# Kernel optimization log

Hardware: AMD Instinct MI355X
Metric: run time of the kernel (lower is better)

Reference implementation:

```python
import jax, jax.numpy as jnp
import numpy as np

PAD = 0  # padding token id; its embedding row is zero (padding_idx)


def setup_inputs() -> dict:
    key = jax.random.key(0)
    k1, k2, k3 = jax.random.split(key, 3)
    HOPS, VOCAB, D = 3, 50257, 128
    B, M, S = 32, 512, 6        # batch, memory slots, tokens per slot
    T, L = 128, 64              # trees per example, tokens per (flattened) tree
    # hop+1 embedding tables, normal(0, 0.1) like the torch init
    C = 0.1 * jax.random.normal(k1, (HOPS + 1, VOCAB, D), dtype=jnp.float32)
    C = C.at[:, PAD].set(0.0)   # padding_idx row = 0
    story = jax.random.randint(k2, (B, M, S), 0, VOCAB, dtype=jnp.int32)
    kb_tokens = jax.random.randint(k3, (B, T, L), 0, VOCAB, dtype=jnp.int32)
    return {"C": C, "story": story, "kb_tokens": kb_tokens}


def reference(C, story, kb_tokens):
    # C: [hops+1, V, D]; story: [B, M, S]; kb_tokens: [B, T, L]
    hops = C.shape[0] - 1
    B = story.shape[0]
    D = C.shape[-1]
    u = jnp.zeros((B, D), dtype=C.dtype)
    for hop in range(hops):
        # key memory: story slots (sum over tokens) + tree memories (sum over
        # all subtree tokens == dfs recursive sum, since PAD embeds to zero)
        m_story_A = jnp.take(C[hop], story, axis=0).sum(axis=2)       # [B,M,D]
        tree_A = jnp.take(C[hop], kb_tokens, axis=0).sum(axis=2)      # [B,T,D]
        m_A = jnp.concatenate([m_story_A, tree_A], axis=1)            # [B,M+T,D]
        prob = jax.nn.softmax(jnp.einsum("bmd,bd->bm", m_A, u), axis=1)
        # value memory with next-hop table
        m_story_C = jnp.take(C[hop + 1], story, axis=0).sum(axis=2)
        tree_C = jnp.take(C[hop + 1], kb_tokens, axis=0).sum(axis=2)
        m_C = jnp.concatenate([m_story_C, tree_C], axis=1)
        o_k = jnp.einsum("bm,bmd->bd", prob, m_C)
        u = u + o_k
    return u
```

## Files before the change

kernel.cpp:

```cpp
#include <hip/hip_runtime.h>
#include <math.h>

constexpr int HOPS  = 3;
constexpr int VOCAB = 50257;
constexpr int DIM   = 128;
constexpr int NB    = 32;
constexpr int NM    = 512;
constexpr int NS    = 6;
constexpr int NT    = 128;
constexpr int NL    = 64;
constexpr int SLOTS = NM + NT;
constexpr size_t TS = (size_t)VOCAB * DIM;
constexpr size_t TABSTRIDE = (size_t)NB * SLOTS * DIM;

constexpr size_t CH_ELEMS = (size_t)VOCAB * 3 * DIM;
constexpr int NE8 = (int)(CH_ELEMS / 8);

typedef _Float16 half8 __attribute__((ext_vector_type(8)));
typedef _Float16 half4 __attribute__((ext_vector_type(4)));

constexpr int CONV_BLOCKS   = 2048;
constexpr int GATHER_BLOCKS = 2048;

__global__ __launch_bounds__(256) void convert_k(
    const float* __restrict__ C, _Float16* __restrict__ Ch)
{
    for (int e8 = blockIdx.x * 256 + threadIdx.x; e8 < NE8; e8 += CONV_BLOCKS * 256) {
        const size_t base = (size_t)e8 * 8;
        const size_t v    = base / 384;
        const int    rem  = (int)(base % 384);
        const int    tab  = rem >> 7;
        const int    d    = rem & 127;
        const float* src = C + (size_t)(1 + tab) * TS + v * DIM + d;
        float4 f0 = *(const float4*)(src);
        float4 f1 = *(const float4*)(src + 4);
        half8 h;
        h[0]=(_Float16)f0.x; h[1]=(_Float16)f0.y; h[2]=(_Float16)f0.z; h[3]=(_Float16)f0.w;
        h[4]=(_Float16)f1.x; h[5]=(_Float16)f1.y; h[6]=(_Float16)f1.z; h[7]=(_Float16)f1.w;
        *(half8*)(Ch + base) = h;
    }
}

__global__ __launch_bounds__(256) void gather_k(
    const _Float16* __restrict__ Ch, const int* __restrict__ story,
    const int* __restrict__ kb, _Float16* __restrict__ msum)
{
    const int wave = threadIdx.x >> 6, lane = threadIdx.x & 63;
    const int q = lane >> 4, l16 = lane & 15;

    if (wave < 2) {
        const int g = blockIdx.x * 2 + wave;
        const int b = g >> 7, tr = g & (NT - 1);

        const int tok = kb[(size_t)g * NL + lane];

        float a0[8] = {0,0,0,0,0,0,0,0};
        float a1[8] = {0,0,0,0,0,0,0,0};
        float a2[8] = {0,0,0,0,0,0,0,0};

        #pragma unroll
        for (int i = 0; i < 16; ++i) {
            const int s = __shfl(tok, (lane & 48) + i);
            const _Float16* p = Ch + (size_t)s * (3 * DIM) + l16 * 8;
            half8 v0 = *(const half8*)(p);
            half8 v1 = *(const half8*)(p + DIM);
            half8 v2 = *(const half8*)(p + 2 * DIM);
            #pragma unroll
            for (int j = 0; j < 8; ++j) {
                a0[j] = fmaf((float)v0[j], 1.0f, a0[j]);
                a1[j] = fmaf((float)v1[j], 1.0f, a1[j]);
                a2[j] = fmaf((float)v2[j], 1.0f, a2[j]);
            }
        }
        #pragma unroll
        for (int j = 0; j < 8; ++j) {
            a0[j] += __shfl_xor(a0[j], 16); a0[j] += __shfl_xor(a0[j], 32);
            a1[j] += __shfl_xor(a1[j], 16); a1[j] += __shfl_xor(a1[j], 32);
            a2[j] += __shfl_xor(a2[j], 16); a2[j] += __shfl_xor(a2[j], 32);
        }
        if (q == 0) {
            half8 h0, h1, h2;
            #pragma unroll
            for (int j = 0; j < 8; ++j) {
                h0[j] = (_Float16)a0[j]; h1[j] = (_Float16)a1[j]; h2[j] = (_Float16)a2[j];
            }
            const size_t o = ((size_t)b * SLOTS + NM + tr) * DIM + l16 * 8;
            *(half8*)(msum + o)                 = h0;
            *(half8*)(msum + o + TABSTRIDE)     = h1;
            *(half8*)(msum + o + 2 * TABSTRIDE) = h2;
        }
    } else {
        const int wbase = blockIdx.x * 8 + (wave - 2) * 4;
        const int* sidx = story + (size_t)wbase * NS;
        const int tokv = (lane < 4 * NS) ? sidx[lane] : 0;

        const int g = wbase + q;
        const int b = g >> 9, slot = g & (NM - 1);

        float a0[8] = {0,0,0,0,0,0,0,0};
        float a1[8] = {0,0,0,0,0,0,0,0};
        float a2[8] = {0,0,0,0,0,0,0,0};

        #pragma unroll
        for (int i = 0; i < NS; ++i) {
            const int s = __shfl(tokv, q * NS + i);
            const _Float16* p = Ch + (size_t)s * (3 * DIM) + l16 * 8;
            half8 v0 = *(const half8*)(p);
            half8 v1 = *(const half8*)(p + DIM);
            half8 v2 = *(const half8*)(p + 2 * DIM);
            #pragma unroll
            for (int j = 0; j < 8; ++j) {
                a0[j] = fmaf((float)v0[j], 1.0f, a0[j]);
                a1[j] = fmaf((float)v1[j], 1.0f, a1[j]);
                a2[j] = fmaf((float)v2[j], 1.0f, a2[j]);
            }
        }
        half8 h0, h1, h2;
        #pragma unroll
        for (int j = 0; j < 8; ++j) {
            h0[j] = (_Float16)a0[j]; h1[j] = (_Float16)a1[j]; h2[j] = (_Float16)a2[j];
        }
        const size_t o = ((size_t)b * SLOTS + slot) * DIM + l16 * 8;
        *(half8*)(msum + o)                 = h0;
        *(half8*)(msum + o + TABSTRIDE)     = h1;
        *(half8*)(msum + o + 2 * TABSTRIDE) = h2;
    }
}

__global__ __launch_bounds__(1024) void hops_fused(
    const _Float16* __restrict__ msum, float* __restrict__ out)
{
    const int b = blockIdx.x, t = threadIdx.x;
    const int rg = t >> 4, l16 = t & 15, wv = t >> 6, ln = t & 63;
    __shared__ float u_s[DIM];
    __shared__ float probs[SLOTS];
    __shared__ float part[64][DIM + 4];
    __shared__ float red[16];

    const _Float16* base = msum + (size_t)b * SLOTS * DIM;
    const int doff = l16 * 8;

    half8 vc[10];

    {
        float acc[8] = {0,0,0,0,0,0,0,0};
        #pragma unroll
        for (int r = 0; r < 10; ++r)
            vc[r] = *(const half8*)(base + (size_t)(rg + 64 * r) * DIM + doff);
        #pragma unroll
        for (int r = 0; r < 10; ++r) {
            #pragma unroll
            for (int j = 0; j < 8; ++j) acc[j] += (float)vc[r][j];
        }
        #pragma unroll
        for (int j = 0; j < 8; ++j) part[rg][doff + j] = acc[j];
        __syncthreads();
        if (t < DIM) {
            float s = 0.f;
            #pragma unroll
            for (int r = 0; r < 64; ++r) s += part[r][t];
            u_s[t] = s * (1.f / SLOTS);
        }
        __syncthreads();
    }

    #pragma unroll
    for (int hop = 1; hop < HOPS; ++hop) {
        float u_reg[8];
        #pragma unroll
        for (int j = 0; j < 8; ++j) u_reg[j] = u_s[doff + j];

        #pragma unroll
        for (int r = 0; r < 10; ++r) {
            const int m = rg + 64 * r;
            float d = 0.f;
            #pragma unroll
            for (int j = 0; j < 8; ++j) d = fmaf((float)vc[r][j], u_reg[j], d);
            d += __shfl_xor(d, 1); d += __shfl_xor(d, 2);
            d += __shfl_xor(d, 4); d += __shfl_xor(d, 8);
            if (l16 == 0) probs[m] = d;
        }
        __syncthreads();

        float s0 = (t < SLOTS) ? probs[t] : -INFINITY;
        float lmax = s0;
        #pragma unroll
        for (int off = 32; off > 0; off >>= 1) lmax = fmaxf(lmax, __shfl_xor(lmax, off));
        if (ln == 0) red[wv] = lmax;
        __syncthreads();
        lmax = red[0];
        #pragma unroll
        for (int r = 1; r < 16; ++r) lmax = fmaxf(lmax, red[r]);
        __syncthreads();
        float e0 = (t < SLOTS) ? expf(s0 - lmax) : 0.f;
        if (t < SLOTS) probs[t] = e0;
        float lsum = e0;
        #pragma unroll
        for (int off = 32; off > 0; off >>= 1) lsum += __shfl_xor(lsum, off);
        if (ln == 0) red[wv] = lsum;
        __syncthreads();
        float tot = red[0];
        #pragma unroll
        for (int r = 1; r < 16; ++r) tot += red[r];
        const float inv = 1.0f / tot;

        const _Float16* mC = base + (size_t)hop * TABSTRIDE;
        float acc[8] = {0,0,0,0,0,0,0,0};
        #pragma unroll
        for (int r = 0; r < 10; ++r) {
            const int m = rg + 64 * r;
            vc[r] = *(const half8*)(mC + (size_t)m * DIM + doff);
            const float p = probs[m];
            #pragma unroll
            for (int j = 0; j < 8; ++j) acc[j] = fmaf(p, (float)vc[r][j], acc[j]);
        }
        __syncthreads();
        #pragma unroll
        for (int j = 0; j < 8; ++j) part[rg][doff + j] = acc[j];
        __syncthreads();
        if (t < DIM) {
            float s = 0.f;
            #pragma unroll
            for (int r = 0; r < 64; ++r) s += part[r][t];
            u_s[t] += s * inv;
        }
        __syncthreads();
    }

    if (t < DIM) out[b * DIM + t] = u_s[t];
}

extern "C" void kernel_launch(void* const* d_in, const int* in_sizes, int n_in,
                              void* d_out, int out_size, void* d_ws, size_t ws_size,
                              hipStream_t stream) {
    const float* C     = (const float*)d_in[0];
    const int*   story = (const int*)d_in[1];
    const int*   kb    = (const int*)d_in[2];
    float*       out   = (float*)d_out;

    _Float16* Ch   = (_Float16*)d_ws;
    _Float16* msum = Ch + CH_ELEMS;

    convert_k<<<CONV_BLOCKS, 256, 0, stream>>>(C, Ch);
    gather_k<<<GATHER_BLOCKS, 256, 0, stream>>>(Ch, story, kb, msum);
    hops_fused<<<NB, 1024, 0, stream>>>(msum, out);
}
```

Baseline: 212.4 us.

## Fuse convert, gather and hop kernels into one cooperative kernel with grid syncs

Merges the three launches into one cooperative kernel of 256 blocks of 1024 threads, separated by grid-wide barriers. Conversion, gather of trees and story slots, and the hop attention phase run in sequence, with the last phase on 32 blocks only. The aim is to remove inter-kernel launch gaps. In exchange it lowers block-level parallelism, adds grid sync costs, and raises register pressure from sharing one kernel at 1024 threads.

```diff
diff --git a/kernel.cpp b/kernel.cpp
--- a/kernel.cpp
+++ b/kernel.cpp
@@ -1,5 +1,8 @@
 #include <hip/hip_runtime.h>
+#include <hip/hip_cooperative_groups.h>
 #include <math.h>
+
+namespace cg = cooperative_groups;
 
 constexpr int HOPS  = 3;
 constexpr int VOCAB = 50257;
@@ -17,15 +20,20 @@
 constexpr int NE8 = (int)(CH_ELEMS / 8);
 
 typedef _Float16 half8 __attribute__((ext_vector_type(8)));
-typedef _Float16 half4 __attribute__((ext_vector_type(4)));
-
-constexpr int CONV_BLOCKS   = 2048;
-constexpr int GATHER_BLOCKS = 2048;
-
-__global__ __launch_bounds__(256) void convert_k(
-    const float* __restrict__ C, _Float16* __restrict__ Ch)
+
+constexpr int GRID = 256;
+
+__global__ __launch_bounds__(1024) void fused_all(
+    const float* __restrict__ C, const int* __restrict__ story,
+    const int* __restrict__ kb, _Float16* __restrict__ Ch,
+    _Float16* __restrict__ msum, float* __restrict__ out)
 {
-    for (int e8 = blockIdx.x * 256 + threadIdx.x; e8 < NE8; e8 += CONV_BLOCKS * 256) {
+    cg::grid_group grid = cg::this_grid();
+    const int t = threadIdx.x;
+    const int wave = t >> 6, lane = t & 63;
+    const int q = lane >> 4, l16 = lane & 15;
+
+    for (int e8 = blockIdx.x * 1024 + t; e8 < NE8; e8 += GRID * 1024) {
         const size_t base = (size_t)e8 * 8;
         const size_t v    = base / 384;
         const int    rem  = (int)(base % 384);
@@ -39,17 +47,11 @@
         h[4]=(_Float16)f1.x; h[5]=(_Float16)f1.y; h[6]=(_Float16)f1.z; h[7]=(_Float16)f1.w;
         *(half8*)(Ch + base) = h;
     }
-}
-
-__global__ __launch_bounds__(256) void gather_k(
-    const _Float16* __restrict__ Ch, const int* __restrict__ story,
-    const int* __restrict__ kb, _Float16* __restrict__ msum)
-{
-    const int wave = threadIdx.x >> 6, lane = threadIdx.x & 63;
-    const int q = lane >> 4, l16 = lane & 15;
-
-    if (wave < 2) {
-        const int g = blockIdx.x * 2 + wave;
+
+    grid.sync();
+
+    {
+        const int g = blockIdx.x * 16 + wave;
         const int b = g >> 7, tr = g & (NT - 1);
 
         const int tok = kb[(size_t)g * NL + lane];
@@ -89,17 +91,17 @@
             *(half8*)(msum + o + TABSTRIDE)     = h1;
             *(half8*)(msum + o + 2 * TABSTRIDE) = h2;
         }
-    } else {
-        const int wbase = blockIdx.x * 8 + (wave - 2) * 4;
+
+        const int wbase = blockIdx.x * 64 + wave * 4;
         const int* sidx = story + (size_t)wbase * NS;
         const int tokv = (lane < 4 * NS) ? sidx[lane] : 0;
 
-        const int g = wbase + q;
-        const int b = g >> 9, slot = g & (NM - 1);
-
-        float a0[8] = {0,0,0,0,0,0,0,0};
-        float a1[8] = {0,0,0,0,0,0,0,0};
-        float a2[8] = {0,0,0,0,0,0,0,0};
+        const int gs = wbase + q;
+        const int bs = gs >> 9, slot = gs & (NM - 1);
+
+        float b0[8] = {0,0,0,0,0,0,0,0};
+        float b1[8] = {0,0,0,0,0,0,0,0};
+        float b2[8] = {0,0,0,0,0,0,0,0};
 
         #pragma unroll
         for (int i = 0; i < NS; ++i) {
@@ -110,124 +112,124 @@
             half8 v2 = *(const half8*)(p + 2 * DIM);
             #pragma unroll
             for (int j = 0; j < 8; ++j) {
-                a0[j] = fmaf((float)v0[j], 1.0f, a0[j]);
-                a1[j] = fmaf((float)v1[j], 1.0f, a1[j]);
-                a2[j] = fmaf((float)v2[j], 1.0f, a2[j]);
+                b0[j] = fmaf((float)v0[j], 1.0f, b0[j]);
+                b1[j] = fmaf((float)v1[j], 1.0f, b1[j]);
+                b2[j] = fmaf((float)v2[j], 1.0f, b2[j]);
             }
         }
         half8 h0, h1, h2;
         #pragma unroll
         for (int j = 0; j < 8; ++j) {
-            h0[j] = (_Float16)a0[j]; h1[j] = (_Float16)a1[j]; h2[j] = (_Float16)a2[j];
-        }
-        const size_t o = ((size_t)b * SLOTS + slot) * DIM + l16 * 8;
+            h0[j] = (_Float16)b0[j]; h1[j] = (_Float16)b1[j]; h2[j] = (_Float16)b2[j];
+        }
+        const size_t o = ((size_t)bs * SLOTS + slot) * DIM + l16 * 8;
         *(half8*)(msum + o)                 = h0;
         *(half8*)(msum + o + TABSTRIDE)     = h1;
         *(half8*)(msum + o + 2 * TABSTRIDE) = h2;
     }
-}
-
-__global__ __launch_bounds__(1024) void hops_fused(
-    const _Float16* __restrict__ msum, float* __restrict__ out)
-{
-    const int b = blockIdx.x, t = threadIdx.x;
-    const int rg = t >> 4, l16 = t & 15, wv = t >> 6, ln = t & 63;
-    __shared__ float u_s[DIM];
-    __shared__ float probs[SLOTS];
-    __shared__ float part[64][DIM + 4];
-    __shared__ float red[16];
-
-    const _Float16* base = msum + (size_t)b * SLOTS * DIM;
-    const int doff = l16 * 8;
-
-    half8 vc[10];
-
-    {
-        float acc[8] = {0,0,0,0,0,0,0,0};
-        #pragma unroll
-        for (int r = 0; r < 10; ++r)
-            vc[r] = *(const half8*)(base + (size_t)(rg + 64 * r) * DIM + doff);
-        #pragma unroll
-        for (int r = 0; r < 10; ++r) {
-            #pragma unroll
-            for (int j = 0; j < 8; ++j) acc[j] += (float)vc[r][j];
-        }
-        #pragma unroll
-        for (int j = 0; j < 8; ++j) part[rg][doff + j] = acc[j];
-        __syncthreads();
-        if (t < DIM) {
-            float s = 0.f;
-            #pragma unroll
-            for (int r = 0; r < 64; ++r) s += part[r][t];
-            u_s[t] = s * (1.f / SLOTS);
-        }
-        __syncthreads();
+
+    grid.sync();
+
+    if (blockIdx.x < NB) {
+        const int b = blockIdx.x;
+        const int rg = t >> 4, wv = t >> 6, ln = t & 63;
+        __shared__ float u_s[DIM];
+        __shared__ float probs[SLOTS];
+        __shared__ float part[64][DIM + 4];
+        __shared__ float red[16];
+
+        const _Float16* base = msum + (size_t)b * SLOTS * DIM;
+        const int doff = l16 * 8;
+
+        half8 vc[10];
+
+        {
+            float acc[8] = {0,0,0,0,0,0,0,0};
+            #pragma unroll
+            for (int r = 0; r < 10; ++r)
+                vc[r] = *(const half8*)(base + (size_t)(rg + 64 * r) * DIM + doff);
+            #pragma unroll
+            for (int r = 0; r < 10; ++r) {
+                #pragma unroll
+                for (int j = 0; j < 8; ++j) acc[j] += (float)vc[r][j];
+            }
+            #pragma unroll
+            for (int j = 0; j < 8; ++j) part[rg][doff + j] = acc[j];
+            __syncthreads();
+            if (t < DIM) {
+                float s = 0.f;
+                #pragma unroll
+                for (int r = 0; r < 64; ++r) s += part[r][t];
+                u_s[t] = s * (1.f / SLOTS);
+            }
+            __syncthreads();
+        }
+
+        #pragma unroll
+        for (int hop = 1; hop < HOPS; ++hop) {
+            float u_reg[8];
+            #pragma unroll
+            for (int j = 0; j < 8; ++j) u_reg[j] = u_s[doff + j];
+
+            #pragma unroll
+            for (int r = 0; r < 10; ++r) {
+                const int m = rg + 64 * r;
+                float d = 0.f;
+                #pragma unroll
+                for (int j = 0; j < 8; ++j) d = fmaf((float)vc[r][j], u_reg[j], d);
+                d += __shfl_xor(d, 1); d += __shfl_xor(d, 2);
+                d += __shfl_xor(d, 4); d += __shfl_xor(d, 8);
+                if (l16 == 0) probs[m] = d;
+            }
+            __syncthreads();
+
+            float s0 = (t < SLOTS) ? probs[t] : -INFINITY;
+            float lmax = s0;
+            #pragma unroll
+            for (int off = 32; off > 0; off >>= 1) lmax = fmaxf(lmax, __shfl_xor(lmax, off));
+            if (ln == 0) red[wv] = lmax;
+            __syncthreads();
+            lmax = red[0];
+            #pragma unroll
+            for (int r = 1; r < 16; ++r) lmax = fmaxf(lmax, red[r]);
+            __syncthreads();
+            float e0 = (t < SLOTS) ? expf(s0 - lmax) : 0.f;
+            if (t < SLOTS) probs[t] = e0;
+            float lsum = e0;
+            #pragma unroll
+            for (int off = 32; off > 0; off >>= 1) lsum += __shfl_xor(lsum, off);
+            if (ln == 0) red[wv] = lsum;
+            __syncthreads();
+            float tot = red[0];
+            #pragma unroll
+            for (int r = 1; r < 16; ++r) tot += red[r];
+            const float inv = 1.0f / tot;
+
+            const _Float16* mC = base + (size_t)hop * TABSTRIDE;
+            float acc[8] = {0,0,0,0,0,0,0,0};
+            #pragma unroll
+            for (int r = 0; r < 10; ++r) {
+                const int m = rg + 64 * r;
+                vc[r] = *(const half8*)(mC + (size_t)m * DIM + doff);
+                const float p = probs[m];
+                #pragma unroll
+                for (int j = 0; j < 8; ++j) acc[j] = fmaf(p, (float)vc[r][j], acc[j]);
+            }
+            __syncthreads();
+            #pragma unroll
+            for (int j = 0; j < 8; ++j) part[rg][doff + j] = acc[j];
+            __syncthreads();
+            if (t < DIM) {
+                float s = 0.f;
+                #pragma unroll
+                for (int r = 0; r < 64; ++r) s += part[r][t];
+                u_s[t] += s * inv;
+            }
+            __syncthreads();
+        }
+
+        if (t < DIM) out[b * DIM + t] = u_s[t];
     }
-
-    #pragma unroll
-    for (int hop = 1; hop < HOPS; ++hop) {
-        float u_reg[8];
-        #pragma unroll
-        for (int j = 0; j < 8; ++j) u_reg[j] = u_s[doff + j];
-
-        #pragma unroll
-        for (int r = 0; r < 10; ++r) {
-            const int m = rg + 64 * r;
-            float d = 0.f;
-            #pragma unroll
-            for (int j = 0; j < 8; ++j) d = fmaf((float)vc[r][j], u_reg[j], d);
-            d += __shfl_xor(d, 1); d += __shfl_xor(d, 2);
-            d += __shfl_xor(d, 4); d += __shfl_xor(d, 8);
-            if (l16 == 0) probs[m] = d;
-        }
-        __syncthreads();
-
-        float s0 = (t < SLOTS) ? probs[t] : -INFINITY;
-        float lmax = s0;
-        #pragma unroll
-        for (int off = 32; off > 0; off >>= 1) lmax = fmaxf(lmax, __shfl_xor(lmax, off));
-        if (ln == 0) red[wv] = lmax;
-        __syncthreads();
-        lmax = red[0];
-        #pragma unroll
-        for (int r = 1; r < 16; ++r) lmax = fmaxf(lmax, red[r]);
-        __syncthreads();
-        float e0 = (t < SLOTS) ? expf(s0 - lmax) : 0.f;
-        if (t < SLOTS) probs[t] = e0;
-        float lsum = e0;
-        #pragma unroll
-        for (int off = 32; off > 0; off >>= 1) lsum += __shfl_xor(lsum, off);
-        if (ln == 0) red[wv] = lsum;
-        __syncthreads();
-        float tot = red[0];
-        #pragma unroll
-        for (int r = 1; r < 16; ++r) tot += red[r];
-        const float inv = 1.0f / tot;
-
-        const _Float16* mC = base + (size_t)hop * TABSTRIDE;
-        float acc[8] = {0,0,0,0,0,0,0,0};
-        #pragma unroll
-        for (int r = 0; r < 10; ++r) {
-            const int m = rg + 64 * r;
-            vc[r] = *(const half8*)(mC + (size_t)m * DIM + doff);
-            const float p = probs[m];
-            #pragma unroll
-            for (int j = 0; j < 8; ++j) acc[j] = fmaf(p, (float)vc[r][j], acc[j]);
-        }
-        __syncthreads();
-        #pragma unroll
-        for (int j = 0; j < 8; ++j) part[rg][doff + j] = acc[j];
-        __syncthreads();
-        if (t < DIM) {
-            float s = 0.f;
-            #pragma unroll
-            for (int r = 0; r < 64; ++r) s += part[r][t];
-            u_s[t] += s * inv;
-        }
-        __syncthreads();
-    }
-
-    if (t < DIM) out[b * DIM + t] = u_s[t];
 }
 
 extern "C" void kernel_launch(void* const* d_in, const int* in_sizes, int n_in,
@@ -241,7 +243,8 @@
     _Float16* Ch   = (_Float16*)d_ws;
     _Float16* msum = Ch + CH_ELEMS;
 
-    convert_k<<<CONV_BLOCKS, 256, 0, stream>>>(C, Ch);
-    gather_k<<<GATHER_BLOCKS, 256, 0, stream>>>(Ch, story, kb, msum);
-    hops_fused<<<NB, 1024, 0, stream>>>(msum, out);
+    void* args[] = { (void*)&C, (void*)&story, (void*)&kb,
+                     (void*)&Ch, (void*)&msum, (void*)&out };
+    hipLaunchCooperativeKernel((void*)fused_all, dim3(GRID), dim3(1024),
+                               args, 0, stream);
 }
```

Measured after the change: 298.9 us. 1.41x slower.

## Split tree and story gathers into separate blocks, halving per-wave tree work

Applied to the files above, without the earlier changes.

The gather kernel previously mixed 2 tree waves (16 tokens per lane group each) with 2 story waves in every block, so the tree waves ran much longer and the story waves idled. Now tree blocks and story blocks are separate. Each tree is split across two waves of 32 tokens, and the two partial sums are combined through shared memory. This is meant to balance wave runtimes and double the parallelism on the long tree gathers, at the cost of a block sync and LDS traffic for the extra reduction.

```diff
diff --git a/kernel.cpp b/kernel.cpp
--- a/kernel.cpp
+++ b/kernel.cpp
@@ -17,10 +17,11 @@
 constexpr int NE8 = (int)(CH_ELEMS / 8);
 
 typedef _Float16 half8 __attribute__((ext_vector_type(8)));
-typedef _Float16 half4 __attribute__((ext_vector_type(4)));
-
-constexpr int CONV_BLOCKS   = 2048;
-constexpr int GATHER_BLOCKS = 2048;
+
+constexpr int CONV_BLOCKS  = 2048;
+constexpr int TREE_BLOCKS  = NB * NT / 2;
+constexpr int STORY_BLOCKS = NB * NM / 16;
+constexpr int GATHER_BLOCKS = TREE_BLOCKS + STORY_BLOCKS;
 
 __global__ __launch_bounds__(256) void convert_k(
     const float* __restrict__ C, _Float16* __restrict__ Ch)
@@ -48,19 +49,21 @@
     const int wave = threadIdx.x >> 6, lane = threadIdx.x & 63;
     const int q = lane >> 4, l16 = lane & 15;
 
-    if (wave < 2) {
-        const int g = blockIdx.x * 2 + wave;
+    if (blockIdx.x < TREE_BLOCKS) {
+        __shared__ float tred[4][3][DIM];
+        const int tl = wave >> 1, half = wave & 1;
+        const int g = blockIdx.x * 2 + tl;
         const int b = g >> 7, tr = g & (NT - 1);
 
-        const int tok = kb[(size_t)g * NL + lane];
+        const int tok = (lane < 32) ? kb[(size_t)g * NL + half * 32 + lane] : 0;
 
         float a0[8] = {0,0,0,0,0,0,0,0};
         float a1[8] = {0,0,0,0,0,0,0,0};
         float a2[8] = {0,0,0,0,0,0,0,0};
 
         #pragma unroll
-        for (int i = 0; i < 16; ++i) {
-            const int s = __shfl(tok, (lane & 48) + i);
+        for (int i = 0; i < 8; ++i) {
+            const int s = __shfl(tok, q * 8 + i);
             const _Float16* p = Ch + (size_t)s * (3 * DIM) + l16 * 8;
             half8 v0 = *(const half8*)(p);
             half8 v1 = *(const half8*)(p + DIM);
@@ -79,10 +82,22 @@
             a2[j] += __shfl_xor(a2[j], 16); a2[j] += __shfl_xor(a2[j], 32);
         }
         if (q == 0) {
+            #pragma unroll
+            for (int j = 0; j < 8; ++j) {
+                tred[wave][0][l16 * 8 + j] = a0[j];
+                tred[wave][1][l16 * 8 + j] = a1[j];
+                tred[wave][2][l16 * 8 + j] = a2[j];
+            }
+        }
+        __syncthreads();
+        if (half == 0 && q == 0) {
             half8 h0, h1, h2;
             #pragma unroll
             for (int j = 0; j < 8; ++j) {
-                h0[j] = (_Float16)a0[j]; h1[j] = (_Float16)a1[j]; h2[j] = (_Float16)a2[j];
+                const int d = l16 * 8 + j;
+                h0[j] = (_Float16)(tred[wave][0][d] + tred[wave + 1][0][d]);
+                h1[j] = (_Float16)(tred[wave][1][d] + tred[wave + 1][1][d]);
+                h2[j] = (_Float16)(tred[wave][2][d] + tred[wave + 1][2][d]);
             }
             const size_t o = ((size_t)b * SLOTS + NM + tr) * DIM + l16 * 8;
             *(half8*)(msum + o)                 = h0;
@@ -90,7 +105,8 @@
             *(half8*)(msum + o + 2 * TABSTRIDE) = h2;
         }
     } else {
-        const int wbase = blockIdx.x * 8 + (wave - 2) * 4;
+        const int sb = blockIdx.x - TREE_BLOCKS;
+        const int wbase = sb * 16 + wave * 4;
         const int* sidx = story + (size_t)wbase * NS;
         const int tokv = (lane < 4 * NS) ? sidx[lane] : 0;
 
```

After: 213.8 us. About the same (+0.6%).

## Partition fp16 embedding copy into 8 dimension slices for cache-local gather

Applied to the files above, without the earlier changes.

The converted fp16 table is re-laid out as 8 slices of 16 dims each ([x][vocab][table][16]). The gather is split so that each block handles one dimension slice, giving each slice about 4.8 MB of table to work on, so it can stay resident in cache. Partial sums are reduced through shared memory. The trade-off is 8x more blocks, shorter 32-byte accesses per token, extra shared-memory reductions and syncs, and redundant token index loads.

```diff
diff --git a/kernel.cpp b/kernel.cpp
--- a/kernel.cpp
+++ b/kernel.cpp
@@ -13,17 +13,21 @@
 constexpr size_t TS = (size_t)VOCAB * DIM;
 constexpr size_t TABSTRIDE = (size_t)NB * SLOTS * DIM;
 
+constexpr int NG = 8;
+constexpr int GW = 16;
 constexpr size_t CH_ELEMS = (size_t)VOCAB * 3 * DIM;
 constexpr int NE8 = (int)(CH_ELEMS / 8);
 
 typedef _Float16 half8 __attribute__((ext_vector_type(8)));
-typedef _Float16 half4 __attribute__((ext_vector_type(4)));
-
-constexpr int CONV_BLOCKS   = 2048;
-constexpr int GATHER_BLOCKS = 2048;
+
+constexpr int CONV_BLOCKS = 2048;
+constexpr int TREE_B2   = NB * NT * NG / 4;
+constexpr int STORY_GB  = (NB * NM + 11) / 12;
+constexpr int STORY_B2  = STORY_GB * NG;
+constexpr int GATHER_B2 = TREE_B2 + STORY_B2;
 
 __global__ __launch_bounds__(256) void convert_k(
-    const float* __restrict__ C, _Float16* __restrict__ Ch)
+    const float* __restrict__ C, _Float16* __restrict__ Ch2)
 {
     for (int e8 = blockIdx.x * 256 + threadIdx.x; e8 < NE8; e8 += CONV_BLOCKS * 256) {
         const size_t base = (size_t)e8 * 8;
@@ -31,99 +35,118 @@
         const int    rem  = (int)(base % 384);
         const int    tab  = rem >> 7;
         const int    d    = rem & 127;
+        const int    x    = d >> 4;
+        const int    dl   = d & 15;
         const float* src = C + (size_t)(1 + tab) * TS + v * DIM + d;
         float4 f0 = *(const float4*)(src);
         float4 f1 = *(const float4*)(src + 4);
         half8 h;
         h[0]=(_Float16)f0.x; h[1]=(_Float16)f0.y; h[2]=(_Float16)f0.z; h[3]=(_Float16)f0.w;
         h[4]=(_Float16)f1.x; h[5]=(_Float16)f1.y; h[6]=(_Float16)f1.z; h[7]=(_Float16)f1.w;
-        *(half8*)(Ch + base) = h;
+        const size_t out = (((size_t)x * VOCAB + v) * 3 + tab) * GW + dl;
+        *(half8*)(Ch2 + out) = h;
     }
 }
 
 __global__ __launch_bounds__(256) void gather_k(
-    const _Float16* __restrict__ Ch, const int* __restrict__ story,
+    const _Float16* __restrict__ Ch2, const int* __restrict__ story,
     const int* __restrict__ kb, _Float16* __restrict__ msum)
 {
+    __shared__ float shm [4][54][17];
+    __shared__ float shm2[4][3][16];
+
     const int wave = threadIdx.x >> 6, lane = threadIdx.x & 63;
-    const int q = lane >> 4, l16 = lane & 15;
-
-    if (wave < 2) {
-        const int g = blockIdx.x * 2 + wave;
+    const int x = blockIdx.x & 7;
+    const _Float16* gbase = Ch2 + (size_t)x * VOCAB * (3 * GW);
+
+    if (blockIdx.x < TREE_B2) {
+        const int g = (blockIdx.x >> 3) * 4 + wave;
         const int b = g >> 7, tr = g & (NT - 1);
 
         const int tok = kb[(size_t)g * NL + lane];
 
-        float a0[8] = {0,0,0,0,0,0,0,0};
-        float a1[8] = {0,0,0,0,0,0,0,0};
-        float a2[8] = {0,0,0,0,0,0,0,0};
-
-        #pragma unroll
-        for (int i = 0; i < 16; ++i) {
-            const int s = __shfl(tok, (lane & 48) + i);
-            const _Float16* p = Ch + (size_t)s * (3 * DIM) + l16 * 8;
-            half8 v0 = *(const half8*)(p);
-            half8 v1 = *(const half8*)(p + DIM);
-            half8 v2 = *(const half8*)(p + 2 * DIM);
+        const int p = lane >> 1, oct = lane & 1;
+        const int tabL = p % 3, kL = p / 3;
+
+        float acc[8] = {0,0,0,0,0,0,0,0};
+        #pragma unroll
+        for (int r = 0; r < 7; ++r) {
+            const int ti = 10 * r + kL;
+            int s = __shfl(tok, ti & 63);
+            if (ti >= 64 || p >= 30) s = 0;
+            const _Float16* ptr = gbase + ((size_t)s * 3 + tabL) * GW + oct * 8;
+            half8 v = *(const half8*)ptr;
+            #pragma unroll
+            for (int j = 0; j < 8; ++j) acc[j] += (float)v[j];
+        }
+        if (p < 30) {
+            #pragma unroll
+            for (int j = 0; j < 8; ++j) shm[wave][p][oct * 8 + j] = acc[j];
+        }
+        __syncthreads();
+        if (lane < 48) {
+            const int tab2 = lane >> 4, d2 = lane & 15;
+            float s = 0.f;
+            #pragma unroll
+            for (int k = 0; k < 10; ++k) s += shm[wave][3 * k + tab2][d2];
+            shm2[wave][tab2][d2] = s;
+        }
+        __syncthreads();
+        if (lane < 6) {
+            const int tab3 = lane >> 1, oct3 = lane & 1;
+            half8 h;
+            #pragma unroll
+            for (int j = 0; j < 8; ++j) h[j] = (_Float16)shm2[wave][tab3][oct3 * 8 + j];
+            const size_t o = ((size_t)b * SLOTS + NM + tr) * DIM + x * GW + oct3 * 8;
+            *(half8*)(msum + o + (size_t)tab3 * TABSTRIDE) = h;
+        }
+    } else {
+        const int gb = (blockIdx.x - TREE_B2) >> 3;
+        const int s0 = gb * 12 + wave * 3;
+        const int rem = NB * NM - s0;
+        const int nv = rem < 0 ? 0 : (rem < 3 ? rem : 3);
+
+        const int tokv = (lane < nv * NS && lane < 18)
+                       ? story[(size_t)s0 * NS + lane] : 0;
+
+        const int p = lane;
+        const int tabL = p % 3, tkL = (p / 3) % 6, slL = p / 18;
+        int s = 0;
+        if (p < 54) s = __shfl(tokv, slL * NS + tkL);
+
+        const _Float16* ptr = gbase + ((size_t)s * 3 + tabL) * GW;
+        half8 v0 = *(const half8*)(ptr);
+        half8 v1 = *(const half8*)(ptr + 8);
+        if (p < 54) {
             #pragma unroll
             for (int j = 0; j < 8; ++j) {
-                a0[j] = fmaf((float)v0[j], 1.0f, a0[j]);
-                a1[j] = fmaf((float)v1[j], 1.0f, a1[j]);
-                a2[j] = fmaf((float)v2[j], 1.0f, a2[j]);
+                shm[wave][p][j]     = (float)v0[j];
+                shm[wave][p][8 + j] = (float)v1[j];
             }
         }
         #pragma unroll
-        for (int j = 0; j < 8; ++j) {
-            a0[j] += __shfl_xor(a0[j], 16); a0[j] += __shfl_xor(a0[j], 32);
-            a1[j] += __shfl_xor(a1[j], 16); a1[j] += __shfl_xor(a1[j], 32);
-            a2[j] += __shfl_xor(a2[j], 16); a2[j] += __shfl_xor(a2[j], 32);
-        }
-        if (q == 0) {
-            half8 h0, h1, h2;
-            #pragma unroll
-            for (int j = 0; j < 8; ++j) {
-                h0[j] = (_Float16)a0[j]; h1[j] = (_Float16)a1[j]; h2[j] = (_Float16)a2[j];
+        for (int s3 = 0; s3 < 3; ++s3) {
+            __syncthreads();
+            if (lane < 48) {
+                const int tab2 = lane >> 4, d2 = lane & 15;
+                float sum = 0.f;
+                #pragma unroll
+                for (int t = 0; t < NS; ++t)
+                    sum += shm[wave][s3 * 18 + t * 3 + tab2][d2];
+                shm2[wave][tab2][d2] = sum;
             }
-            const size_t o = ((size_t)b * SLOTS + NM + tr) * DIM + l16 * 8;
-            *(half8*)(msum + o)                 = h0;
-            *(half8*)(msum + o + TABSTRIDE)     = h1;
-            *(half8*)(msum + o + 2 * TABSTRIDE) = h2;
-        }
-    } else {
-        const int wbase = blockIdx.x * 8 + (wave - 2) * 4;
-        const int* sidx = story + (size_t)wbase * NS;
-        const int tokv = (lane < 4 * NS) ? sidx[lane] : 0;
-
-        const int g = wbase + q;
-        const int b = g >> 9, slot = g & (NM - 1);
-
-        float a0[8] = {0,0,0,0,0,0,0,0};
-        float a1[8] = {0,0,0,0,0,0,0,0};
-        float a2[8] = {0,0,0,0,0,0,0,0};
-
-        #pragma unroll
-        for (int i = 0; i < NS; ++i) {
-            const int s = __shfl(tokv, q * NS + i);
-            const _Float16* p = Ch + (size_t)s * (3 * DIM) + l16 * 8;
-            half8 v0 = *(const half8*)(p);
-            half8 v1 = *(const half8*)(p + DIM);
-            half8 v2 = *(const half8*)(p + 2 * DIM);
-            #pragma unroll
-            for (int j = 0; j < 8; ++j) {
-                a0[j] = fmaf((float)v0[j], 1.0f, a0[j]);
-                a1[j] = fmaf((float)v1[j], 1.0f, a1[j]);
-                a2[j] = fmaf((float)v2[j], 1.0f, a2[j]);
+            __syncthreads();
+            if (lane < 6 && s3 < nv) {
+                const int tab3 = lane >> 1, oct3 = lane & 1;
+                const int sg = s0 + s3;
+                const int bb = sg >> 9, sl = sg & (NM - 1);
+                half8 h;
+                #pragma unroll
+                for (int j = 0; j < 8; ++j) h[j] = (_Float16)shm2[wave][tab3][oct3 * 8 + j];
+                const size_t o = ((size_t)bb * SLOTS + sl) * DIM + x * GW + oct3 * 8;
+                *(half8*)(msum + o + (size_t)tab3 * TABSTRIDE) = h;
             }
         }
-        half8 h0, h1, h2;
-        #pragma unroll
-        for (int j = 0; j < 8; ++j) {
-            h0[j] = (_Float16)a0[j]; h1[j] = (_Float16)a1[j]; h2[j] = (_Float16)a2[j];
-        }
-        const size_t o = ((size_t)b * SLOTS + slot) * DIM + l16 * 8;
-        *(half8*)(msum + o)                 = h0;
-        *(half8*)(msum + o + TABSTRIDE)     = h1;
-        *(half8*)(msum + o + 2 * TABSTRIDE) = h2;
     }
 }
 
@@ -238,10 +261,10 @@
     const int*   kb    = (const int*)d_in[2];
     float*       out   = (float*)d_out;
 
-    _Float16* Ch   = (_Float16*)d_ws;
-    _Float16* msum = Ch + CH_ELEMS;
-
-    convert_k<<<CONV_BLOCKS, 256, 0, stream>>>(C, Ch);
-    gather_k<<<GATHER_BLOCKS, 256, 0, stream>>>(Ch, story, kb, msum);
+    _Float16* Ch2  = (_Float16*)d_ws;
+    _Float16* msum = Ch2 + CH_ELEMS;
+
+    convert_k<<<CONV_BLOCKS, 256, 0, stream>>>(C, Ch2);
+    gather_k<<<GATHER_B2, 256, 0, stream>>>(Ch2, story, kb, msum);
     hops_fused<<<NB, 1024, 0, stream>>>(msum, out);
 }
```

Result: no change. 216.3 us (+1.8%).
